# Kernel tuning notes

Measured on AMD Instinct MI355X. Metric: run time of the kernel, lower is better.

The kernel has to match this reference:

```python
import jax, jax.numpy as jnp
import numpy as np

DIM = 512
NUM_HEADS = 8
HEAD_DIM = DIM // NUM_HEADS
B, S = 2, 2048


def setup_inputs() -> dict:
    key = jax.random.key(0)
    ks = jax.random.split(key, 16)
    scale = 1.0 / np.sqrt(DIM)
    inp = {
        "x": jax.random.normal(ks[0], (B, S, DIM), dtype=jnp.float32),
        "Qexpl": jax.random.normal(ks[1], (B, S, DIM), dtype=jnp.float32),
        "Kexpl": jax.random.normal(ks[2], (B, S, DIM), dtype=jnp.float32),
        "fl": jax.random.uniform(ks[3], (B,), dtype=jnp.float32),
        "fu": jax.random.uniform(ks[4], (B,), dtype=jnp.float32),
        "age": jax.random.uniform(ks[5], (B,), dtype=jnp.float32),
        "gender": jax.random.uniform(ks[6], (B,), dtype=jnp.float32),
        # Linear params: weight stored as [out, in] like torch; y = x @ W.T + b
        "Wq": jax.random.normal(ks[7], (DIM, DIM), dtype=jnp.float32) * scale,
        "bq": jnp.zeros((DIM,), dtype=jnp.float32),
        "Wk": jax.random.normal(ks[8], (DIM, DIM), dtype=jnp.float32) * scale,
        "bk": jnp.zeros((DIM,), dtype=jnp.float32),
        "Wv": jax.random.normal(ks[9], (DIM, DIM), dtype=jnp.float32) * scale,
        "bv": jnp.zeros((DIM,), dtype=jnp.float32),
        "Wo": jax.random.normal(ks[10], (DIM, DIM), dtype=jnp.float32) * scale,
        "bo": jnp.zeros((DIM,), dtype=jnp.float32),
    }
    return inp


def reference(x, Qexpl, Kexpl, fl, fu, age, gender, Wq, bq, Wk, bk, Wv, bv, Wo, bo):
    # drofe_fn is None -> Q/K projections used directly.
    Q = Qexpl @ Wq.T + bq            # [B, S, D]
    K = Kexpl @ Wk.T + bk            # [B, S, D]
    V = x @ Wv.T + bv                # [B, S, D]

    def split_heads(t):  # [B, S, D] -> [B, H, S, hd]
        return t.reshape(B, S, NUM_HEADS, HEAD_DIM).transpose(0, 2, 1, 3)

    Qh, Kh, Vh = split_heads(Q), split_heads(K), split_heads(V)
    scale = 1.0 / np.sqrt(HEAD_DIM).astype(np.float32)
    scores = jnp.einsum("bhqd,bhkd->bhqk", Qh, Kh) * scale  # [B, H, S, S]
    weights = jax.nn.softmax(scores, axis=-1)
    attn = jnp.einsum("bhqk,bhkd->bhqd", weights, Vh)        # [B, H, S, hd]
    attn = attn.transpose(0, 2, 1, 3).reshape(B, S, DIM)
    return attn @ Wo.T + bo
```

## Files before the change

### kernel.cpp

```cpp
#include <hip/hip_runtime.h>
#include <hip/hip_bf16.h>

typedef unsigned short ushort_t;
typedef __attribute__((ext_vector_type(8))) short bf16x8;
typedef __attribute__((ext_vector_type(4))) float f32x4;

__device__ __forceinline__ ushort_t f2bf(float f) {
    union { float f; unsigned u; } v; v.f = f;
    unsigned r = v.u + 0x7FFF + ((v.u >> 16) & 1);
    return (ushort_t)(r >> 16);
}
__device__ __forceinline__ bf16x8 ld8(const ushort_t* p) { return *(const bf16x8*)p; }

__device__ __forceinline__ unsigned cvt2(float x, float y) {
    __hip_bfloat162 h = __float22bfloat162_rn(make_float2(x, y));
    unsigned r; __builtin_memcpy(&r, &h, 4); return r;
}
__device__ __forceinline__ bf16x8 pack8f(float4 a, float4 b) {
    union { unsigned u[4]; bf16x8 v; } o;
    o.u[0] = cvt2(a.x, a.y); o.u[1] = cvt2(a.z, a.w);
    o.u[2] = cvt2(b.x, b.y); o.u[3] = cvt2(b.z, b.w);
    return o.v;
}

struct CvtArgs { const float* src[4]; ushort_t* dst[4]; };

__global__ __launch_bounds__(256)
void cvt_kernel(CvtArgs a) {
    const int seg = blockIdx.y;
    const float* s = a.src[seg];
    ushort_t* d = a.dst[seg];
    int i = (blockIdx.x * 256 + threadIdx.x) * 8;
    float4 x = *(const float4*)(s + i);
    float4 y = *(const float4*)(s + i + 4);
    union { unsigned u[4]; ushort4 v[2]; } o;
    o.u[0] = cvt2(x.x, x.y); o.u[1] = cvt2(x.z, x.w);
    o.u[2] = cvt2(y.x, y.y); o.u[3] = cvt2(y.z, y.w);
    *(ushort4*)(d + i) = o.v[0];
    *(ushort4*)(d + i + 4) = o.v[1];
}

__global__ __launch_bounds__(256, 3)
void proj_qkv_kernel(const float* __restrict__ Qe, const float* __restrict__ Ke,
                     const float* __restrict__ x,
                     const ushort_t* __restrict__ Wq, const ushort_t* __restrict__ Wk,
                     const ushort_t* __restrict__ Wv,
                     const float* __restrict__ bq, const float* __restrict__ bk,
                     const float* __restrict__ bv,
                     ushort_t* __restrict__ Qo, ushort_t* __restrict__ Ko,
                     ushort_t* __restrict__ Vt)
{
    __shared__ ushort_t lA[64 * 72];
    __shared__ ushort_t lB[128 * 72];
    const int z = blockIdx.z;
    const float* A = (z == 0) ? Qe : (z == 1) ? Ke : x;
    const ushort_t* W = (z == 0) ? Wq : (z == 1) ? Wk : Wv;
    const float* bias = (z == 0) ? bq : (z == 1) ? bk : bv;

    const int m0 = blockIdx.y * 64, n0 = blockIdx.x * 128;
    const int t = threadIdx.x;
    const int lane = t & 63, wave = t >> 6;
    const int wm = (wave & 1) * 32, wn = (wave >> 1) * 64;
    const int fr = lane & 15, quad = lane >> 4;

    f32x4 acc[2][4] = {};
    float4 fa[2][2];
    bf16x8 vb[4];

#pragma unroll
    for (int i = 0; i < 2; ++i) {
        int s = i * 256 + t;
        int r = s >> 3, jp = s & 7;
        const float* p = A + (size_t)(m0 + r) * 512 + jp * 8;
        fa[i][0] = *(const float4*)p;
        fa[i][1] = *(const float4*)(p + 4);
    }
#pragma unroll
    for (int i = 0; i < 4; ++i) {
        int s = i * 256 + t;
        int r = s >> 3, jp = s & 7;
        vb[i] = ld8(W + (size_t)(n0 + r) * 512 + jp * 8);
    }

    for (int kk = 0; kk < 8; ++kk) {
        if (kk) __syncthreads();
#pragma unroll
        for (int i = 0; i < 2; ++i) {
            int s = i * 256 + t;
            int r = s >> 3, jp = s & 7;
            *(bf16x8*)(lA + r * 72 + jp * 8) = pack8f(fa[i][0], fa[i][1]);
        }
#pragma unroll
        for (int i = 0; i < 4; ++i) {
            int s = i * 256 + t;
            int r = s >> 3, jp = s & 7;
            *(bf16x8*)(lB + r * 72 + jp * 8) = vb[i];
        }
        __syncthreads();
        if (kk < 7) {
            int k0 = (kk + 1) * 64;
#pragma unroll
            for (int i = 0; i < 2; ++i) {
                int s = i * 256 + t;
                int r = s >> 3, jp = s & 7;
                const float* p = A + (size_t)(m0 + r) * 512 + k0 + jp * 8;
                fa[i][0] = *(const float4*)p;
                fa[i][1] = *(const float4*)(p + 4);
            }
#pragma unroll
            for (int i = 0; i < 4; ++i) {
                int s = i * 256 + t;
                int r = s >> 3, jp = s & 7;
                vb[i] = ld8(W + (size_t)(n0 + r) * 512 + k0 + jp * 8);
            }
        }

        bf16x8 af[2][2], bfrag[4][2];
#pragma unroll
        for (int ks = 0; ks < 2; ++ks) {
#pragma unroll
            for (int mt = 0; mt < 2; ++mt)
                af[mt][ks] = ld8(lA + (wm + mt * 16 + fr) * 72 + (ks * 4 + quad) * 8);
#pragma unroll
            for (int nt = 0; nt < 4; ++nt)
                bfrag[nt][ks] = ld8(lB + (wn + nt * 16 + fr) * 72 + (ks * 4 + quad) * 8);
        }
#pragma unroll
        for (int ks = 0; ks < 2; ++ks)
#pragma unroll
            for (int mt = 0; mt < 2; ++mt)
#pragma unroll
                for (int nt = 0; nt < 4; ++nt)
                    acc[mt][nt] = __builtin_amdgcn_mfma_f32_16x16x32_bf16(
                        af[mt][ks], bfrag[nt][ks], acc[mt][nt], 0, 0, 0);
    }

    const float C1 = 0.125f * 1.44269504088896340736f;
#pragma unroll
    for (int nt = 0; nt < 4; ++nt) {
        int n = n0 + wn + nt * 16 + fr;
        float bb = bias[n];
#pragma unroll
        for (int mt = 0; mt < 2; ++mt) {
            int mb = m0 + wm + mt * 16 + quad * 4;
            if (z == 0) {
#pragma unroll
                for (int r = 0; r < 4; ++r)
                    Qo[(size_t)(mb + r) * 512 + n] = f2bf((acc[mt][nt][r] + bb) * C1);
            } else if (z == 1) {
#pragma unroll
                for (int r = 0; r < 4; ++r)
                    Ko[(size_t)(mb + r) * 512 + n] = f2bf(acc[mt][nt][r] + bb);
            } else {
                int h = n >> 6, d = n & 63;
                int bidx = mb >> 11;
                int st = mb & 2047;
                int a = (st >> 4) & 7;
                size_t base = ((size_t)((bidx * 8 + h) * 64 + d)) * 2048 + (st & ~127) + a;
#pragma unroll
                for (int r = 0; r < 4; ++r)
                    Vt[base + (size_t)(quad * 4 + r) * 8] = f2bf(acc[mt][nt][r] + bb);
            }
        }
    }
}

__global__ __launch_bounds__(256, 2)
void gemm_o_kernel(const ushort_t* __restrict__ A, const ushort_t* __restrict__ W,
                   const float* __restrict__ bias, float* __restrict__ dst)
{
    __shared__ ushort_t lA[64 * 72];
    __shared__ ushort_t lB[64 * 72];
    const int m0 = blockIdx.y * 64, n0 = blockIdx.x * 64;
    const int t = threadIdx.x;
    const int lane = t & 63, wave = t >> 6;
    const int wm = (wave & 1) * 32, wn = (wave >> 1) * 32;
    const int fr = lane & 15, quad = lane >> 4;

    f32x4 acc[2][2] = {};
    bf16x8 va[2], vb[2];

#pragma unroll
    for (int i = 0; i < 2; ++i) {
        int s = i * 256 + t;
        int r = s >> 3, jp = s & 7;
        va[i] = ld8(A + (size_t)(m0 + r) * 512 + jp * 8);
        vb[i] = ld8(W + (size_t)(n0 + r) * 512 + jp * 8);
    }

    for (int kk = 0; kk < 8; ++kk) {
        if (kk) __syncthreads();
#pragma unroll
        for (int i = 0; i < 2; ++i) {
            int s = i * 256 + t;
            int r = s >> 3, jp = s & 7;
            *(bf16x8*)(lA + r * 72 + jp * 8) = va[i];
            *(bf16x8*)(lB + r * 72 + jp * 8) = vb[i];
        }
        __syncthreads();
        if (kk < 7) {
            int k0 = (kk + 1) * 64;
#pragma unroll
            for (int i = 0; i < 2; ++i) {
                int s = i * 256 + t;
                int r = s >> 3, jp = s & 7;
                va[i] = ld8(A + (size_t)(m0 + r) * 512 + k0 + jp * 8);
                vb[i] = ld8(W + (size_t)(n0 + r) * 512 + k0 + jp * 8);
            }
        }

        bf16x8 af[2][2], bfrag[2][2];
#pragma unroll
        for (int ks = 0; ks < 2; ++ks) {
#pragma unroll
            for (int mt = 0; mt < 2; ++mt)
                af[mt][ks] = ld8(lA + (wm + mt * 16 + fr) * 72 + (ks * 4 + quad) * 8);
#pragma unroll
            for (int nt = 0; nt < 2; ++nt)
                bfrag[nt][ks] = ld8(lB + (wn + nt * 16 + fr) * 72 + (ks * 4 + quad) * 8);
        }
#pragma unroll
        for (int ks = 0; ks < 2; ++ks)
#pragma unroll
            for (int mt = 0; mt < 2; ++mt)
#pragma unroll
                for (int nt = 0; nt < 2; ++nt)
                    acc[mt][nt] = __builtin_amdgcn_mfma_f32_16x16x32_bf16(
                        af[mt][ks], bfrag[nt][ks], acc[mt][nt], 0, 0, 0);
    }

#pragma unroll
    for (int nt = 0; nt < 2; ++nt) {
        int n = n0 + wn + nt * 16 + fr;
        float bb = bias[n];
#pragma unroll
        for (int mt = 0; mt < 2; ++mt) {
            int mb = m0 + wm + mt * 16 + quad * 4;
#pragma unroll
            for (int r = 0; r < 4; ++r)
                dst[(size_t)(mb + r) * 512 + n] = acc[mt][nt][r] + bb;
        }
    }
}

__global__ __launch_bounds__(256, 2)
void attn_kernel(const ushort_t* __restrict__ Q, const ushort_t* __restrict__ K,
                 const ushort_t* __restrict__ Vt, ushort_t* __restrict__ O)
{
    __shared__ ushort_t lK[128 * 72];
    __shared__ ushort_t lVt[64 * 136];
    __shared__ ushort_t lP[64 * 136];

    const int b = blockIdx.z, h = blockIdx.y;
    const int q0 = blockIdx.x * 64;
    const int t = threadIdx.x;
    const int lane = t & 63, wave = t >> 6;
    const int wq = wave * 16;
    const int fr = lane & 15, quad = lane >> 4;

    bf16x8 aq[2];
    {
        const ushort_t* qp = Q + (size_t)(b * 2048 + q0 + wq + fr) * 512 + h * 64 + quad * 8;
        aq[0] = ld8(qp);
        aq[1] = ld8(qp + 32);
    }

    f32x4 oacc[4] = {};
    float lpart[4] = {};
    bf16x8 vk[4], vv[4];

#pragma unroll
    for (int i = 0; i < 4; ++i) {
        int s = i * 256 + t;
        int r = s >> 3, jp = s & 7;
        vk[i] = ld8(K + (size_t)(b * 2048 + r) * 512 + h * 64 + jp * 8);
        int r2 = s >> 4, jp2 = s & 15;
        vv[i] = ld8(Vt + (size_t)((b * 8 + h) * 64 + r2) * 2048 + jp2 * 8);
    }

    for (int kv = 0; kv < 2048; kv += 128) {
        if (kv) __syncthreads();
#pragma unroll
        for (int i = 0; i < 4; ++i) {
            int s = i * 256 + t;
            int r = s >> 3, jp = s & 7;
            *(bf16x8*)(lK + r * 72 + jp * 8) = vk[i];
            int r2 = s >> 4, jp2 = s & 15;
            *(bf16x8*)(lVt + r2 * 136 + jp2 * 8) = vv[i];
        }
        __syncthreads();
        if (kv + 128 < 2048) {
            int kn = kv + 128;
#pragma unroll
            for (int i = 0; i < 4; ++i) {
                int s = i * 256 + t;
                int r = s >> 3, jp = s & 7;
                vk[i] = ld8(K + (size_t)(b * 2048 + kn + r) * 512 + h * 64 + jp * 8);
                int r2 = s >> 4, jp2 = s & 15;
                vv[i] = ld8(Vt + (size_t)((b * 8 + h) * 64 + r2) * 2048 + kn + jp2 * 8);
            }
        }

        f32x4 sc[8] = {};
#pragma unroll
        for (int ks = 0; ks < 2; ++ks)
#pragma unroll
            for (int nt = 0; nt < 8; ++nt) {
                bf16x8 kb = ld8(lK + (nt * 16 + fr) * 72 + (ks * 4 + quad) * 8);
                sc[nt] = __builtin_amdgcn_mfma_f32_16x16x32_bf16(aq[ks], kb, sc[nt], 0, 0, 0);
            }

#pragma unroll
        for (int r = 0; r < 4; ++r) {
            int row = wq + quad * 4 + r;
            float pv[8];
            float acc = 0.f;
#pragma unroll
            for (int nt = 0; nt < 8; ++nt) {
                pv[nt] = exp2f(sc[nt][r]);
                acc += pv[nt];
            }
            lpart[r] += acc;
            union { unsigned u[4]; bf16x8 v; } pu;
            pu.u[0] = cvt2(pv[0], pv[1]); pu.u[1] = cvt2(pv[2], pv[3]);
            pu.u[2] = cvt2(pv[4], pv[5]); pu.u[3] = cvt2(pv[6], pv[7]);
            *(bf16x8*)(lP + row * 136 + fr * 8) = pu.v;
        }

#pragma unroll
        for (int ks = 0; ks < 4; ++ks) {
            bf16x8 ap = ld8(lP + (wq + fr) * 136 + ks * 32 + quad * 8);
#pragma unroll
            for (int nt = 0; nt < 4; ++nt) {
                bf16x8 vb = ld8(lVt + (nt * 16 + fr) * 136 + ks * 32 + quad * 8);
                oacc[nt] = __builtin_amdgcn_mfma_f32_16x16x32_bf16(ap, vb, oacc[nt], 0, 0, 0);
            }
        }
    }

#pragma unroll
    for (int r = 0; r < 4; ++r) {
        float rs = lpart[r];
#pragma unroll
        for (int o = 1; o < 16; o <<= 1)
            rs += __shfl_xor(rs, o, 64);
        float inv = 1.f / rs;
        int q = q0 + wq + quad * 4 + r;
#pragma unroll
        for (int nt = 0; nt < 4; ++nt) {
            int d = nt * 16 + fr;
            O[(size_t)(b * 2048 + q) * 512 + h * 64 + d] = f2bf(oacc[nt][r] * inv);
        }
    }
}

extern "C" void kernel_launch(void* const* d_in, const int* in_sizes, int n_in,
                              void* d_out, int out_size, void* d_ws, size_t ws_size,
                              hipStream_t stream) {
    const float* x   = (const float*)d_in[0];
    const float* Qe  = (const float*)d_in[1];
    const float* Ke  = (const float*)d_in[2];
    const float* Wq  = (const float*)d_in[7];
    const float* bq  = (const float*)d_in[8];
    const float* Wk  = (const float*)d_in[9];
    const float* bk  = (const float*)d_in[10];
    const float* Wv  = (const float*)d_in[11];
    const float* bv  = (const float*)d_in[12];
    const float* Wo  = (const float*)d_in[13];
    const float* bo  = (const float*)d_in[14];

    const size_t NTOK = 2 * 2048;
    const size_t ACT = NTOK * 512;
    const size_t WSZ = 512 * 512;

    ushort_t* p = (ushort_t*)d_ws;
    ushort_t* Wqb = p; p += WSZ;
    ushort_t* Wkb = p; p += WSZ;
    ushort_t* Wvb = p; p += WSZ;
    ushort_t* Wob = p; p += WSZ;
    ushort_t* Qws = p; p += ACT;
    ushort_t* Kws = p; p += ACT;
    ushort_t* Vt  = p; p += ACT;
    ushort_t* Ows = p; p += ACT;

    CvtArgs ca;
    ca.src[0] = Wq; ca.dst[0] = Wqb;
    ca.src[1] = Wk; ca.dst[1] = Wkb;
    ca.src[2] = Wv; ca.dst[2] = Wvb;
    ca.src[3] = Wo; ca.dst[3] = Wob;
    cvt_kernel<<<dim3(128, 4), 256, 0, stream>>>(ca);

    proj_qkv_kernel<<<dim3(4, 64, 3), 256, 0, stream>>>(Qe, Ke, x, Wqb, Wkb, Wvb,
                                                        bq, bk, bv, Qws, Kws, Vt);
    attn_kernel<<<dim3(32, 8, 2), 256, 0, stream>>>(Qws, Kws, Vt, Ows);
    gemm_o_kernel<<<dim3(8, 64), 256, 0, stream>>>(Ows, Wob, bo, (float*)d_out);
}
```

Before: 168.8 us.

## Fuse weight bf16 conversion into GEMMs and give attention waves two query tiles

Drops the separate weight-conversion kernel. The projection and output GEMMs now load fp32 weights directly and pack them to bf16 while staging into shared memory, which removes one launch and a workspace round trip at the cost of twice the weight bytes read per tile. The attention kernel moves to 128 threads per block, with each wave owning 32 query rows (two 16-row MFMA tiles), so each K/V shared-memory fragment is reused across two tiles. Halving the block size means fewer waves share the K/V staging, and register pressure per wave increases.

```diff
diff --git a/kernel.cpp b/kernel.cpp
--- a/kernel.cpp
+++ b/kernel.cpp
@@ -23,28 +23,11 @@
     return o.v;
 }
 
-struct CvtArgs { const float* src[4]; ushort_t* dst[4]; };
-
-__global__ __launch_bounds__(256)
-void cvt_kernel(CvtArgs a) {
-    const int seg = blockIdx.y;
-    const float* s = a.src[seg];
-    ushort_t* d = a.dst[seg];
-    int i = (blockIdx.x * 256 + threadIdx.x) * 8;
-    float4 x = *(const float4*)(s + i);
-    float4 y = *(const float4*)(s + i + 4);
-    union { unsigned u[4]; ushort4 v[2]; } o;
-    o.u[0] = cvt2(x.x, x.y); o.u[1] = cvt2(x.z, x.w);
-    o.u[2] = cvt2(y.x, y.y); o.u[3] = cvt2(y.z, y.w);
-    *(ushort4*)(d + i) = o.v[0];
-    *(ushort4*)(d + i + 4) = o.v[1];
-}
-
 __global__ __launch_bounds__(256, 3)
 void proj_qkv_kernel(const float* __restrict__ Qe, const float* __restrict__ Ke,
                      const float* __restrict__ x,
-                     const ushort_t* __restrict__ Wq, const ushort_t* __restrict__ Wk,
-                     const ushort_t* __restrict__ Wv,
+                     const float* __restrict__ Wq, const float* __restrict__ Wk,
+                     const float* __restrict__ Wv,
                      const float* __restrict__ bq, const float* __restrict__ bk,
                      const float* __restrict__ bv,
                      ushort_t* __restrict__ Qo, ushort_t* __restrict__ Ko,
@@ -54,7 +37,7 @@
     __shared__ ushort_t lB[128 * 72];
     const int z = blockIdx.z;
     const float* A = (z == 0) ? Qe : (z == 1) ? Ke : x;
-    const ushort_t* W = (z == 0) ? Wq : (z == 1) ? Wk : Wv;
+    const float* W = (z == 0) ? Wq : (z == 1) ? Wk : Wv;
     const float* bias = (z == 0) ? bq : (z == 1) ? bk : bv;
 
     const int m0 = blockIdx.y * 64, n0 = blockIdx.x * 128;
@@ -64,22 +47,21 @@
     const int fr = lane & 15, quad = lane >> 4;
 
     f32x4 acc[2][4] = {};
-    float4 fa[2][2];
-    bf16x8 vb[4];
+    float4 fa[2][2], fw[4][2];
 
 #pragma unroll
     for (int i = 0; i < 2; ++i) {
         int s = i * 256 + t;
         int r = s >> 3, jp = s & 7;
         const float* p = A + (size_t)(m0 + r) * 512 + jp * 8;
-        fa[i][0] = *(const float4*)p;
-        fa[i][1] = *(const float4*)(p + 4);
+        fa[i][0] = *(const float4*)p; fa[i][1] = *(const float4*)(p + 4);
     }
 #pragma unroll
     for (int i = 0; i < 4; ++i) {
         int s = i * 256 + t;
         int r = s >> 3, jp = s & 7;
-        vb[i] = ld8(W + (size_t)(n0 + r) * 512 + jp * 8);
+        const float* p = W + (size_t)(n0 + r) * 512 + jp * 8;
+        fw[i][0] = *(const float4*)p; fw[i][1] = *(const float4*)(p + 4);
     }
 
     for (int kk = 0; kk < 8; ++kk) {
@@ -94,7 +76,7 @@
         for (int i = 0; i < 4; ++i) {
             int s = i * 256 + t;
             int r = s >> 3, jp = s & 7;
-            *(bf16x8*)(lB + r * 72 + jp * 8) = vb[i];
+            *(bf16x8*)(lB + r * 72 + jp * 8) = pack8f(fw[i][0], fw[i][1]);
         }
         __syncthreads();
         if (kk < 7) {
@@ -104,14 +86,14 @@
                 int s = i * 256 + t;
                 int r = s >> 3, jp = s & 7;
                 const float* p = A + (size_t)(m0 + r) * 512 + k0 + jp * 8;
-                fa[i][0] = *(const float4*)p;
-                fa[i][1] = *(const float4*)(p + 4);
+                fa[i][0] = *(const float4*)p; fa[i][1] = *(const float4*)(p + 4);
             }
 #pragma unroll
             for (int i = 0; i < 4; ++i) {
                 int s = i * 256 + t;
                 int r = s >> 3, jp = s & 7;
-                vb[i] = ld8(W + (size_t)(n0 + r) * 512 + k0 + jp * 8);
+                const float* p = W + (size_t)(n0 + r) * 512 + k0 + jp * 8;
+                fw[i][0] = *(const float4*)p; fw[i][1] = *(const float4*)(p + 4);
             }
         }
 
@@ -166,7 +148,7 @@
 }
 
 __global__ __launch_bounds__(256, 2)
-void gemm_o_kernel(const ushort_t* __restrict__ A, const ushort_t* __restrict__ W,
+void gemm_o_kernel(const ushort_t* __restrict__ A, const float* __restrict__ W,
                    const float* __restrict__ bias, float* __restrict__ dst)
 {
     __shared__ ushort_t lA[64 * 72];
@@ -178,14 +160,16 @@
     const int fr = lane & 15, quad = lane >> 4;
 
     f32x4 acc[2][2] = {};
-    bf16x8 va[2], vb[2];
+    bf16x8 va[2];
+    float4 fw[2][2];
 
 #pragma unroll
     for (int i = 0; i < 2; ++i) {
         int s = i * 256 + t;
         int r = s >> 3, jp = s & 7;
         va[i] = ld8(A + (size_t)(m0 + r) * 512 + jp * 8);
-        vb[i] = ld8(W + (size_t)(n0 + r) * 512 + jp * 8);
+        const float* p = W + (size_t)(n0 + r) * 512 + jp * 8;
+        fw[i][0] = *(const float4*)p; fw[i][1] = *(const float4*)(p + 4);
     }
 
     for (int kk = 0; kk < 8; ++kk) {
@@ -195,7 +179,7 @@
             int s = i * 256 + t;
             int r = s >> 3, jp = s & 7;
             *(bf16x8*)(lA + r * 72 + jp * 8) = va[i];
-            *(bf16x8*)(lB + r * 72 + jp * 8) = vb[i];
+            *(bf16x8*)(lB + r * 72 + jp * 8) = pack8f(fw[i][0], fw[i][1]);
         }
         __syncthreads();
         if (kk < 7) {
@@ -205,7 +189,8 @@
                 int s = i * 256 + t;
                 int r = s >> 3, jp = s & 7;
                 va[i] = ld8(A + (size_t)(m0 + r) * 512 + k0 + jp * 8);
-                vb[i] = ld8(W + (size_t)(n0 + r) * 512 + k0 + jp * 8);
+                const float* p = W + (size_t)(n0 + r) * 512 + k0 + jp * 8;
+                fw[i][0] = *(const float4*)p; fw[i][1] = *(const float4*)(p + 4);
             }
         }
 
@@ -243,7 +228,7 @@
     }
 }
 
-__global__ __launch_bounds__(256, 2)
+__global__ __launch_bounds__(128, 2)
 void attn_kernel(const ushort_t* __restrict__ Q, const ushort_t* __restrict__ K,
                  const ushort_t* __restrict__ Vt, ushort_t* __restrict__ O)
 {
@@ -255,23 +240,25 @@
     const int q0 = blockIdx.x * 64;
     const int t = threadIdx.x;
     const int lane = t & 63, wave = t >> 6;
-    const int wq = wave * 16;
+    const int wq = wave * 32;
     const int fr = lane & 15, quad = lane >> 4;
 
-    bf16x8 aq[2];
-    {
-        const ushort_t* qp = Q + (size_t)(b * 2048 + q0 + wq + fr) * 512 + h * 64 + quad * 8;
-        aq[0] = ld8(qp);
-        aq[1] = ld8(qp + 32);
-    }
-
-    f32x4 oacc[4] = {};
-    float lpart[4] = {};
-    bf16x8 vk[4], vv[4];
-
-#pragma unroll
-    for (int i = 0; i < 4; ++i) {
-        int s = i * 256 + t;
+    bf16x8 aq[2][2];
+#pragma unroll
+    for (int mt = 0; mt < 2; ++mt) {
+        const ushort_t* qp = Q + (size_t)(b * 2048 + q0 + wq + mt * 16 + fr) * 512
+                             + h * 64 + quad * 8;
+        aq[mt][0] = ld8(qp);
+        aq[mt][1] = ld8(qp + 32);
+    }
+
+    f32x4 oacc[2][4] = {};
+    float lpart[2][4] = {};
+    bf16x8 vk[8], vv[8];
+
+#pragma unroll
+    for (int i = 0; i < 8; ++i) {
+        int s = i * 128 + t;
         int r = s >> 3, jp = s & 7;
         vk[i] = ld8(K + (size_t)(b * 2048 + r) * 512 + h * 64 + jp * 8);
         int r2 = s >> 4, jp2 = s & 15;
@@ -281,8 +268,8 @@
     for (int kv = 0; kv < 2048; kv += 128) {
         if (kv) __syncthreads();
 #pragma unroll
-        for (int i = 0; i < 4; ++i) {
-            int s = i * 256 + t;
+        for (int i = 0; i < 8; ++i) {
+            int s = i * 128 + t;
             int r = s >> 3, jp = s & 7;
             *(bf16x8*)(lK + r * 72 + jp * 8) = vk[i];
             int r2 = s >> 4, jp2 = s & 15;
@@ -292,8 +279,8 @@
         if (kv + 128 < 2048) {
             int kn = kv + 128;
 #pragma unroll
-            for (int i = 0; i < 4; ++i) {
-                int s = i * 256 + t;
+            for (int i = 0; i < 8; ++i) {
+                int s = i * 128 + t;
                 int r = s >> 3, jp = s & 7;
                 vk[i] = ld8(K + (size_t)(b * 2048 + kn + r) * 512 + h * 64 + jp * 8);
                 int r2 = s >> 4, jp2 = s & 15;
@@ -301,57 +288,70 @@
             }
         }
 
-        f32x4 sc[8] = {};
+        f32x4 sc[2][8] = {};
 #pragma unroll
         for (int ks = 0; ks < 2; ++ks)
 #pragma unroll
             for (int nt = 0; nt < 8; ++nt) {
                 bf16x8 kb = ld8(lK + (nt * 16 + fr) * 72 + (ks * 4 + quad) * 8);
-                sc[nt] = __builtin_amdgcn_mfma_f32_16x16x32_bf16(aq[ks], kb, sc[nt], 0, 0, 0);
-            }
-
-#pragma unroll
-        for (int r = 0; r < 4; ++r) {
-            int row = wq + quad * 4 + r;
-            float pv[8];
-            float acc = 0.f;
-#pragma unroll
-            for (int nt = 0; nt < 8; ++nt) {
-                pv[nt] = exp2f(sc[nt][r]);
-                acc += pv[nt];
-            }
-            lpart[r] += acc;
-            union { unsigned u[4]; bf16x8 v; } pu;
-            pu.u[0] = cvt2(pv[0], pv[1]); pu.u[1] = cvt2(pv[2], pv[3]);
-            pu.u[2] = cvt2(pv[4], pv[5]); pu.u[3] = cvt2(pv[6], pv[7]);
-            *(bf16x8*)(lP + row * 136 + fr * 8) = pu.v;
-        }
+#pragma unroll
+                for (int mt = 0; mt < 2; ++mt)
+                    sc[mt][nt] = __builtin_amdgcn_mfma_f32_16x16x32_bf16(
+                        aq[mt][ks], kb, sc[mt][nt], 0, 0, 0);
+            }
+
+#pragma unroll
+        for (int mt = 0; mt < 2; ++mt)
+#pragma unroll
+            for (int r = 0; r < 4; ++r) {
+                int row = wq + mt * 16 + quad * 4 + r;
+                float pv[8];
+                float acc = 0.f;
+#pragma unroll
+                for (int nt = 0; nt < 8; ++nt) {
+                    pv[nt] = exp2f(sc[mt][nt][r]);
+                    acc += pv[nt];
+                }
+                lpart[mt][r] += acc;
+                union { unsigned u[4]; bf16x8 v; } pu;
+                pu.u[0] = cvt2(pv[0], pv[1]); pu.u[1] = cvt2(pv[2], pv[3]);
+                pu.u[2] = cvt2(pv[4], pv[5]); pu.u[3] = cvt2(pv[6], pv[7]);
+                *(bf16x8*)(lP + row * 136 + fr * 8) = pu.v;
+            }
 
 #pragma unroll
         for (int ks = 0; ks < 4; ++ks) {
-            bf16x8 ap = ld8(lP + (wq + fr) * 136 + ks * 32 + quad * 8);
+            bf16x8 ap[2];
+#pragma unroll
+            for (int mt = 0; mt < 2; ++mt)
+                ap[mt] = ld8(lP + (wq + mt * 16 + fr) * 136 + ks * 32 + quad * 8);
 #pragma unroll
             for (int nt = 0; nt < 4; ++nt) {
                 bf16x8 vb = ld8(lVt + (nt * 16 + fr) * 136 + ks * 32 + quad * 8);
-                oacc[nt] = __builtin_amdgcn_mfma_f32_16x16x32_bf16(ap, vb, oacc[nt], 0, 0, 0);
-            }
-        }
-    }
-
-#pragma unroll
-    for (int r = 0; r < 4; ++r) {
-        float rs = lpart[r];
-#pragma unroll
-        for (int o = 1; o < 16; o <<= 1)
-            rs += __shfl_xor(rs, o, 64);
-        float inv = 1.f / rs;
-        int q = q0 + wq + quad * 4 + r;
-#pragma unroll
-        for (int nt = 0; nt < 4; ++nt) {
-            int d = nt * 16 + fr;
-            O[(size_t)(b * 2048 + q) * 512 + h * 64 + d] = f2bf(oacc[nt][r] * inv);
-        }
-    }
+#pragma unroll
+                for (int mt = 0; mt < 2; ++mt)
+                    oacc[mt][nt] = __builtin_amdgcn_mfma_f32_16x16x32_bf16(
+                        ap[mt], vb, oacc[mt][nt], 0, 0, 0);
+            }
+        }
+    }
+
+#pragma unroll
+    for (int mt = 0; mt < 2; ++mt)
+#pragma unroll
+        for (int r = 0; r < 4; ++r) {
+            float rs = lpart[mt][r];
+#pragma unroll
+            for (int o = 1; o < 16; o <<= 1)
+                rs += __shfl_xor(rs, o, 64);
+            float inv = 1.f / rs;
+            int q = q0 + wq + mt * 16 + quad * 4 + r;
+#pragma unroll
+            for (int nt = 0; nt < 4; ++nt) {
+                int d = nt * 16 + fr;
+                O[(size_t)(b * 2048 + q) * 512 + h * 64 + d] = f2bf(oacc[mt][nt][r] * inv);
+            }
+        }
 }
 
 extern "C" void kernel_launch(void* const* d_in, const int* in_sizes, int n_in,
@@ -371,27 +371,15 @@
 
     const size_t NTOK = 2 * 2048;
     const size_t ACT = NTOK * 512;
-    const size_t WSZ = 512 * 512;
 
     ushort_t* p = (ushort_t*)d_ws;
-    ushort_t* Wqb = p; p += WSZ;
-    ushort_t* Wkb = p; p += WSZ;
-    ushort_t* Wvb = p; p += WSZ;
-    ushort_t* Wob = p; p += WSZ;
     ushort_t* Qws = p; p += ACT;
     ushort_t* Kws = p; p += ACT;
     ushort_t* Vt  = p; p += ACT;
     ushort_t* Ows = p; p += ACT;
 
-    CvtArgs ca;
-    ca.src[0] = Wq; ca.dst[0] = Wqb;
-    ca.src[1] = Wk; ca.dst[1] = Wkb;
-    ca.src[2] = Wv; ca.dst[2] = Wvb;
-    ca.src[3] = Wo; ca.dst[3] = Wob;
-    cvt_kernel<<<dim3(128, 4), 256, 0, stream>>>(ca);
-
-    proj_qkv_kernel<<<dim3(4, 64, 3), 256, 0, stream>>>(Qe, Ke, x, Wqb, Wkb, Wvb,
+    proj_qkv_kernel<<<dim3(4, 64, 3), 256, 0, stream>>>(Qe, Ke, x, Wq, Wk, Wv,
                                                         bq, bk, bv, Qws, Kws, Vt);
-    attn_kernel<<<dim3(32, 8, 2), 256, 0, stream>>>(Qws, Kws, Vt, Ows);
-    gemm_o_kernel<<<dim3(8, 64), 256, 0, stream>>>(Ows, Wob, bo, (float*)d_out);
-}
+    attn_kernel<<<dim3(32, 8, 2), 128, 0, stream>>>(Qws, Kws, Vt, Ows);
+    gemm_o_kernel<<<dim3(8, 64), 256, 0, stream>>>(Ows, Wo, bo, (float*)d_out);
+}
```

Measured after the change: 213.6 us. 26.5% more time.

## Fuse weight bf16 conversion into GEMMs, enlarge QKV tile, stage V transpose via LDS

Applied to the files above, without the earlier changes.

Drops the separate weight-conversion kernel and instead loads fp32 weights inside the projection and output GEMMs, packing them to bf16 as they are staged into LDS. The QKV projection tile grows from 64x128 to 128x128, so each wave computes 4x4 MFMA tiles. The transposed V output is now staged through LDS and written as 16-byte vector stores instead of scattered 2-byte stores. This saves one launch and reuses weight loads across a larger M tile, at the cost of redundant weight conversion in every block, higher register pressure (occupancy hint lowered to 2), and fewer QKV blocks.

```diff
diff --git a/kernel.cpp b/kernel.cpp
--- a/kernel.cpp
+++ b/kernel.cpp
@@ -23,150 +23,140 @@
     return o.v;
 }
 
-struct CvtArgs { const float* src[4]; ushort_t* dst[4]; };
-
-__global__ __launch_bounds__(256)
-void cvt_kernel(CvtArgs a) {
-    const int seg = blockIdx.y;
-    const float* s = a.src[seg];
-    ushort_t* d = a.dst[seg];
-    int i = (blockIdx.x * 256 + threadIdx.x) * 8;
-    float4 x = *(const float4*)(s + i);
-    float4 y = *(const float4*)(s + i + 4);
-    union { unsigned u[4]; ushort4 v[2]; } o;
-    o.u[0] = cvt2(x.x, x.y); o.u[1] = cvt2(x.z, x.w);
-    o.u[2] = cvt2(y.x, y.y); o.u[3] = cvt2(y.z, y.w);
-    *(ushort4*)(d + i) = o.v[0];
-    *(ushort4*)(d + i + 4) = o.v[1];
-}
-
-__global__ __launch_bounds__(256, 3)
+__global__ __launch_bounds__(256, 2)
 void proj_qkv_kernel(const float* __restrict__ Qe, const float* __restrict__ Ke,
                      const float* __restrict__ x,
-                     const ushort_t* __restrict__ Wq, const ushort_t* __restrict__ Wk,
-                     const ushort_t* __restrict__ Wv,
+                     const float* __restrict__ Wq, const float* __restrict__ Wk,
+                     const float* __restrict__ Wv,
                      const float* __restrict__ bq, const float* __restrict__ bk,
                      const float* __restrict__ bv,
                      ushort_t* __restrict__ Qo, ushort_t* __restrict__ Ko,
                      ushort_t* __restrict__ Vt)
 {
-    __shared__ ushort_t lA[64 * 72];
-    __shared__ ushort_t lB[128 * 72];
+    __shared__ ushort_t smem[2 * 128 * 72];
+    ushort_t* lA = smem;
+    ushort_t* lB = smem + 128 * 72;
+
     const int z = blockIdx.z;
     const float* A = (z == 0) ? Qe : (z == 1) ? Ke : x;
-    const ushort_t* W = (z == 0) ? Wq : (z == 1) ? Wk : Wv;
+    const float* W = (z == 0) ? Wq : (z == 1) ? Wk : Wv;
     const float* bias = (z == 0) ? bq : (z == 1) ? bk : bv;
 
-    const int m0 = blockIdx.y * 64, n0 = blockIdx.x * 128;
+    const int m0 = blockIdx.y * 128, n0 = blockIdx.x * 128;
     const int t = threadIdx.x;
     const int lane = t & 63, wave = t >> 6;
-    const int wm = (wave & 1) * 32, wn = (wave >> 1) * 64;
+    const int wm = (wave & 1) * 64, wn = (wave >> 1) * 64;
     const int fr = lane & 15, quad = lane >> 4;
 
-    f32x4 acc[2][4] = {};
-    float4 fa[2][2];
-    bf16x8 vb[4];
-
-#pragma unroll
-    for (int i = 0; i < 2; ++i) {
-        int s = i * 256 + t;
-        int r = s >> 3, jp = s & 7;
-        const float* p = A + (size_t)(m0 + r) * 512 + jp * 8;
-        fa[i][0] = *(const float4*)p;
-        fa[i][1] = *(const float4*)(p + 4);
-    }
+    f32x4 acc[4][4] = {};
+    float4 fa[4][2], fw[4][2];
+
 #pragma unroll
     for (int i = 0; i < 4; ++i) {
         int s = i * 256 + t;
         int r = s >> 3, jp = s & 7;
-        vb[i] = ld8(W + (size_t)(n0 + r) * 512 + jp * 8);
+        const float* pa = A + (size_t)(m0 + r) * 512 + jp * 8;
+        fa[i][0] = *(const float4*)pa; fa[i][1] = *(const float4*)(pa + 4);
+        const float* pw = W + (size_t)(n0 + r) * 512 + jp * 8;
+        fw[i][0] = *(const float4*)pw; fw[i][1] = *(const float4*)(pw + 4);
     }
 
     for (int kk = 0; kk < 8; ++kk) {
         if (kk) __syncthreads();
 #pragma unroll
-        for (int i = 0; i < 2; ++i) {
+        for (int i = 0; i < 4; ++i) {
             int s = i * 256 + t;
             int r = s >> 3, jp = s & 7;
             *(bf16x8*)(lA + r * 72 + jp * 8) = pack8f(fa[i][0], fa[i][1]);
-        }
-#pragma unroll
-        for (int i = 0; i < 4; ++i) {
-            int s = i * 256 + t;
-            int r = s >> 3, jp = s & 7;
-            *(bf16x8*)(lB + r * 72 + jp * 8) = vb[i];
+            *(bf16x8*)(lB + r * 72 + jp * 8) = pack8f(fw[i][0], fw[i][1]);
         }
         __syncthreads();
         if (kk < 7) {
             int k0 = (kk + 1) * 64;
-#pragma unroll
-            for (int i = 0; i < 2; ++i) {
-                int s = i * 256 + t;
-                int r = s >> 3, jp = s & 7;
-                const float* p = A + (size_t)(m0 + r) * 512 + k0 + jp * 8;
-                fa[i][0] = *(const float4*)p;
-                fa[i][1] = *(const float4*)(p + 4);
-            }
 #pragma unroll
             for (int i = 0; i < 4; ++i) {
                 int s = i * 256 + t;
                 int r = s >> 3, jp = s & 7;
-                vb[i] = ld8(W + (size_t)(n0 + r) * 512 + k0 + jp * 8);
-            }
-        }
-
-        bf16x8 af[2][2], bfrag[4][2];
+                const float* pa = A + (size_t)(m0 + r) * 512 + k0 + jp * 8;
+                fa[i][0] = *(const float4*)pa; fa[i][1] = *(const float4*)(pa + 4);
+                const float* pw = W + (size_t)(n0 + r) * 512 + k0 + jp * 8;
+                fw[i][0] = *(const float4*)pw; fw[i][1] = *(const float4*)(pw + 4);
+            }
+        }
+
 #pragma unroll
         for (int ks = 0; ks < 2; ++ks) {
-#pragma unroll
-            for (int mt = 0; mt < 2; ++mt)
-                af[mt][ks] = ld8(lA + (wm + mt * 16 + fr) * 72 + (ks * 4 + quad) * 8);
+            bf16x8 af[4], bfrag[4];
+#pragma unroll
+            for (int mt = 0; mt < 4; ++mt)
+                af[mt] = ld8(lA + (wm + mt * 16 + fr) * 72 + (ks * 4 + quad) * 8);
 #pragma unroll
             for (int nt = 0; nt < 4; ++nt)
-                bfrag[nt][ks] = ld8(lB + (wn + nt * 16 + fr) * 72 + (ks * 4 + quad) * 8);
-        }
-#pragma unroll
-        for (int ks = 0; ks < 2; ++ks)
-#pragma unroll
-            for (int mt = 0; mt < 2; ++mt)
+                bfrag[nt] = ld8(lB + (wn + nt * 16 + fr) * 72 + (ks * 4 + quad) * 8);
+#pragma unroll
+            for (int mt = 0; mt < 4; ++mt)
 #pragma unroll
                 for (int nt = 0; nt < 4; ++nt)
                     acc[mt][nt] = __builtin_amdgcn_mfma_f32_16x16x32_bf16(
-                        af[mt][ks], bfrag[nt][ks], acc[mt][nt], 0, 0, 0);
+                        af[mt], bfrag[nt], acc[mt][nt], 0, 0, 0);
+        }
     }
 
     const float C1 = 0.125f * 1.44269504088896340736f;
-#pragma unroll
-    for (int nt = 0; nt < 4; ++nt) {
-        int n = n0 + wn + nt * 16 + fr;
-        float bb = bias[n];
-#pragma unroll
-        for (int mt = 0; mt < 2; ++mt) {
-            int mb = m0 + wm + mt * 16 + quad * 4;
-            if (z == 0) {
-#pragma unroll
-                for (int r = 0; r < 4; ++r)
-                    Qo[(size_t)(mb + r) * 512 + n] = f2bf((acc[mt][nt][r] + bb) * C1);
-            } else if (z == 1) {
-#pragma unroll
-                for (int r = 0; r < 4; ++r)
-                    Ko[(size_t)(mb + r) * 512 + n] = f2bf(acc[mt][nt][r] + bb);
-            } else {
-                int h = n >> 6, d = n & 63;
-                int bidx = mb >> 11;
-                int st = mb & 2047;
-                int a = (st >> 4) & 7;
-                size_t base = ((size_t)((bidx * 8 + h) * 64 + d)) * 2048 + (st & ~127) + a;
-#pragma unroll
-                for (int r = 0; r < 4; ++r)
-                    Vt[base + (size_t)(quad * 4 + r) * 8] = f2bf(acc[mt][nt][r] + bb);
-            }
+    if (z != 2) {
+        ushort_t* dst = (z == 0) ? Qo : Ko;
+#pragma unroll
+        for (int nt = 0; nt < 4; ++nt) {
+            int n = n0 + wn + nt * 16 + fr;
+            float bb = bias[n];
+#pragma unroll
+            for (int mt = 0; mt < 4; ++mt) {
+                int mb = m0 + wm + mt * 16 + quad * 4;
+                if (z == 0) {
+#pragma unroll
+                    for (int r = 0; r < 4; ++r)
+                        dst[(size_t)(mb + r) * 512 + n] = f2bf((acc[mt][nt][r] + bb) * C1);
+                } else {
+#pragma unroll
+                    for (int r = 0; r < 4; ++r)
+                        dst[(size_t)(mb + r) * 512 + n] = f2bf(acc[mt][nt][r] + bb);
+                }
+            }
+        }
+    } else {
+        __syncthreads();
+        ushort_t* lT = smem;
+#pragma unroll
+        for (int nt = 0; nt < 4; ++nt) {
+            int nl = wn + nt * 16 + fr;
+            float bb = bias[n0 + nl];
+#pragma unroll
+            for (int mt = 0; mt < 4; ++mt) {
+                int tm = wm + mt * 16 + quad * 4;
+#pragma unroll
+                for (int r = 0; r < 4; ++r) {
+                    int tl = tm + r;
+                    int sg = 8 * (tl & 15) + ((tl >> 4) & 7);
+                    lT[nl * 136 + sg] = f2bf(acc[mt][nt][r] + bb);
+                }
+            }
+        }
+        __syncthreads();
+        const int bidx = m0 >> 11, m0t = m0 & 2047;
+#pragma unroll
+        for (int i = 0; i < 8; ++i) {
+            int s = i * 256 + t;
+            int row = s >> 4, c = s & 15;
+            int n = n0 + row;
+            int h = n >> 6, d = n & 63;
+            bf16x8 v = ld8(lT + row * 136 + c * 8);
+            *(bf16x8*)(Vt + ((size_t)((bidx * 8 + h) * 64 + d)) * 2048 + m0t + c * 8) = v;
         }
     }
 }
 
 __global__ __launch_bounds__(256, 2)
-void gemm_o_kernel(const ushort_t* __restrict__ A, const ushort_t* __restrict__ W,
+void gemm_o_kernel(const ushort_t* __restrict__ A, const float* __restrict__ W,
                    const float* __restrict__ bias, float* __restrict__ dst)
 {
     __shared__ ushort_t lA[64 * 72];
@@ -178,14 +168,16 @@
     const int fr = lane & 15, quad = lane >> 4;
 
     f32x4 acc[2][2] = {};
-    bf16x8 va[2], vb[2];
+    bf16x8 va[2];
+    float4 fw[2][2];
 
 #pragma unroll
     for (int i = 0; i < 2; ++i) {
         int s = i * 256 + t;
         int r = s >> 3, jp = s & 7;
         va[i] = ld8(A + (size_t)(m0 + r) * 512 + jp * 8);
-        vb[i] = ld8(W + (size_t)(n0 + r) * 512 + jp * 8);
+        const float* p = W + (size_t)(n0 + r) * 512 + jp * 8;
+        fw[i][0] = *(const float4*)p; fw[i][1] = *(const float4*)(p + 4);
     }
 
     for (int kk = 0; kk < 8; ++kk) {
@@ -195,7 +187,7 @@
             int s = i * 256 + t;
             int r = s >> 3, jp = s & 7;
             *(bf16x8*)(lA + r * 72 + jp * 8) = va[i];
-            *(bf16x8*)(lB + r * 72 + jp * 8) = vb[i];
+            *(bf16x8*)(lB + r * 72 + jp * 8) = pack8f(fw[i][0], fw[i][1]);
         }
         __syncthreads();
         if (kk < 7) {
@@ -205,7 +197,8 @@
                 int s = i * 256 + t;
                 int r = s >> 3, jp = s & 7;
                 va[i] = ld8(A + (size_t)(m0 + r) * 512 + k0 + jp * 8);
-                vb[i] = ld8(W + (size_t)(n0 + r) * 512 + k0 + jp * 8);
+                const float* p = W + (size_t)(n0 + r) * 512 + k0 + jp * 8;
+                fw[i][0] = *(const float4*)p; fw[i][1] = *(const float4*)(p + 4);
             }
         }
 
@@ -371,27 +364,15 @@
 
     const size_t NTOK = 2 * 2048;
     const size_t ACT = NTOK * 512;
-    const size_t WSZ = 512 * 512;
 
     ushort_t* p = (ushort_t*)d_ws;
-    ushort_t* Wqb = p; p += WSZ;
-    ushort_t* Wkb = p; p += WSZ;
-    ushort_t* Wvb = p; p += WSZ;
-    ushort_t* Wob = p; p += WSZ;
     ushort_t* Qws = p; p += ACT;
     ushort_t* Kws = p; p += ACT;
     ushort_t* Vt  = p; p += ACT;
     ushort_t* Ows = p; p += ACT;
 
-    CvtArgs ca;
-    ca.src[0] = Wq; ca.dst[0] = Wqb;
-    ca.src[1] = Wk; ca.dst[1] = Wkb;
-    ca.src[2] = Wv; ca.dst[2] = Wvb;
-    ca.src[3] = Wo; ca.dst[3] = Wob;
-    cvt_kernel<<<dim3(128, 4), 256, 0, stream>>>(ca);
-
-    proj_qkv_kernel<<<dim3(4, 64, 3), 256, 0, stream>>>(Qe, Ke, x, Wqb, Wkb, Wvb,
+    proj_qkv_kernel<<<dim3(4, 32, 3), 256, 0, stream>>>(Qe, Ke, x, Wq, Wk, Wv,
                                                         bq, bk, bv, Qws, Kws, Vt);
     attn_kernel<<<dim3(32, 8, 2), 256, 0, stream>>>(Qws, Kws, Vt, Ows);
-    gemm_o_kernel<<<dim3(8, 64), 256, 0, stream>>>(Ows, Wob, bo, (float*)d_out);
-}
+    gemm_o_kernel<<<dim3(8, 64), 256, 0, stream>>>(Ows, Wo, bo, (float*)d_out);
+}
```

Measured after the change: 167.9 us. No clear change (-0.5%).
